# Kernel optimization log

Measured on AMD Instinct MI355X. Metric: run time of the kernel, lower is better.

## Reference

```python
import jax, jax.numpy as jnp
import numpy as np

N_HEAD = 16
N_FEAT = 1024
D_HEAD = N_FEAT // N_HEAD


def setup_inputs() -> dict:
    key = jax.random.key(0)
    ks = jax.random.split(key, 12)
    B, L, T = 8, 128, 64
    s = 0.05
    return {
        "q": jax.random.normal(ks[0], (B, 1, N_FEAT), jnp.float32),
        "kv": jax.random.normal(ks[1], (B, L, T, N_FEAT), jnp.float32),
        "Wq": jax.random.normal(ks[2], (D_HEAD, D_HEAD), jnp.float32) * s,
        "bq": jax.random.normal(ks[3], (D_HEAD,), jnp.float32) * s,
        "Wk": jax.random.normal(ks[4], (D_HEAD, D_HEAD), jnp.float32) * s,
        "bk": jax.random.normal(ks[5], (D_HEAD,), jnp.float32) * s,
        "Wv": jax.random.normal(ks[6], (D_HEAD, D_HEAD), jnp.float32) * s,
        "bv": jax.random.normal(ks[7], (D_HEAD,), jnp.float32) * s,
        "Wo": jax.random.normal(ks[8], (N_FEAT, N_FEAT), jnp.float32) * s,
        "bo": jax.random.normal(ks[9], (N_FEAT,), jnp.float32) * s,
    }


def reference(q, kv, Wq, bq, Wk, bk, Wv, bv, Wo, bo):
    B, L, T, D = kv.shape
    H, dh = N_HEAD, D_HEAD
    # mean-pool q over its singleton length dim and kv over T for keys
    qm = q.mean(axis=-2)                      # [B, D]
    km = kv.mean(axis=-2)                     # [B, L, D]
    qh = qm.reshape(B, H, dh)                 # [B, H, dh]
    kh = km.reshape(B, L, H, dh)              # [B, L, H, dh]
    vh = kv.reshape(B, L, T, H, dh)           # [B, L, T, H, dh]
    # per-head linear projections (torch Linear: x @ W.T + b)
    qh = qh @ Wq.T + bq
    kh = kh @ Wk.T + bk
    vh = vh @ Wv.T + bv
    # faithful transpose chain from the original module
    qh = jnp.swapaxes(qh, -2, -3)             # [H, B, dh]  (3D: swaps B and H)
    kh = jnp.swapaxes(kh, -2, -3)             # [B, H, L, dh]
    # broadcasted matmul -> cross-batch attention [B, H, B, L]
    attw = jnp.matmul(qh, jnp.swapaxes(kh, -1, -2)) / jnp.sqrt(jnp.float32(dh))
    attn = jax.nn.softmax(attw, axis=-1)      # [B, H, B, L]
    # value reshuffle: [B,L,T,H,dh] -> [B,H,T,L,dh] -> [B,H,T,dh,L] -> [B,H,T*dh,L]
    v = jnp.swapaxes(vh, -2, -4)
    v = jnp.swapaxes(v, -1, -2)
    v = v.reshape(B, H, T * dh, L)
    ct = jnp.matmul(attn, jnp.swapaxes(v, -1, -2))   # [B, H, B, T*dh]
    ct = ct.reshape(B, H, B, T, dh)
    ct = jnp.swapaxes(ct, -2, -4)                    # [B, T, B, H, dh]
    ct = ct.reshape(B, T, B, H * dh)                 # [B, T, B, D]
    return ct @ Wo.T + bo
```

## Files before the change

kernel.cpp:

```cpp
#include <hip/hip_runtime.h>
#include <hip/hip_bf16.h>

#define BDIM 8
#define LDIM 128
#define TDIM 64
#define NFEAT 1024
#define HNUM 16
#define DH 64

#define GM 4096
#define GN 1024
#define GK 1024

typedef __attribute__((ext_vector_type(8))) short short8;
typedef __attribute__((ext_vector_type(4))) float f32x4;

__device__ __forceinline__ unsigned short f2bf(float x) {
  union { float f; unsigned u; } v; v.f = x;
  unsigned r = v.u + 0x7fffu + ((v.u >> 16) & 1u);
  return (unsigned short)(r >> 16);
}

__device__ __forceinline__ void gload_lds16(const void* g, void* l) {
  __builtin_amdgcn_global_load_lds((const __attribute__((address_space(1))) void*)g,
                                   (__attribute__((address_space(3))) void*)l, 16, 0, 0);
}

__global__ __launch_bounds__(256) void mean_score_weff_kernel(
    const float* __restrict__ kv, const float* __restrict__ q,
    const float* __restrict__ Wq, const float* __restrict__ bq,
    const float* __restrict__ Wk, const float* __restrict__ Wo,
    const float* __restrict__ Wv, const float* __restrict__ bv,
    const float* __restrict__ bo, float* __restrict__ scores,
    unsigned short* __restrict__ Weff, float* __restrict__ beff) {
  __shared__ float km_s[NFEAT];
  __shared__ float Wk_s[DH * 67];
  __shared__ float kw_s[HNUM * DH];
  __shared__ float wqkw_s[HNUM * 66];
  __shared__ float bqkw_s[HNUM];
  __shared__ float worow[NFEAT];
  __shared__ float red[256];
  const int bl = blockIdx.x;
  const int tid = threadIdx.x;
  const int b1 = bl >> 7, l = bl & 127;

  {
    const float* src = kv + (size_t)bl * (TDIM * NFEAT) + tid * 4;
    float4 acc = make_float4(0.f, 0.f, 0.f, 0.f);
    for (int t0 = 0; t0 < TDIM; t0 += 8) {
      float4 v[8];
#pragma unroll
      for (int jj = 0; jj < 8; ++jj)
        v[jj] = *(const float4*)(src + (t0 + jj) * NFEAT);
#pragma unroll
      for (int jj = 0; jj < 8; ++jj) {
        acc.x += v[jj].x; acc.y += v[jj].y; acc.z += v[jj].z; acc.w += v[jj].w;
      }
    }
    const float s = 1.f / TDIM;
    *(float4*)(km_s + tid * 4) = make_float4(acc.x * s, acc.y * s, acc.z * s, acc.w * s);
  }
#pragma unroll
  for (int rep = 0; rep < 4; ++rep) {
    const int e4 = rep * 256 + tid;
    const int row = e4 >> 4, c4 = e4 & 15;
    const float4 v = *(const float4*)(Wk + row * DH + c4 * 4);
    float* dst = Wk_s + row * 67 + c4 * 4;
    dst[0] = v.x; dst[1] = v.y; dst[2] = v.z; dst[3] = v.w;
  }
  __syncthreads();
#pragma unroll
  for (int rep = 0; rep < 4; ++rep) {
    const int e = rep * 256 + tid;
    const int h = e >> 6, dd = e & 63;
    float acc = 0.f;
#pragma unroll 4
    for (int d = 0; d < DH; ++d) acc += Wk_s[dd * 67 + d] * km_s[h * 64 + d];
    kw_s[h * 64 + dd] = acc;
  }
  __syncthreads();
#pragma unroll
  for (int rep = 0; rep < 4; ++rep) {
    const int e = rep * 256 + tid;
    const int h = e >> 6, i = e & 63;
    float acc = 0.f;
#pragma unroll 4
    for (int dd = 0; dd < DH; ++dd) acc += Wq[dd * DH + i] * kw_s[h * 64 + dd];
    wqkw_s[h * 66 + i] = acc;
  }
  if (tid < HNUM) {
    float acc = 0.f;
#pragma unroll 4
    for (int dd = 0; dd < DH; ++dd) acc += bq[dd] * kw_s[tid * 64 + dd];
    bqkw_s[tid] = acc;
  }
  __syncthreads();
  if (tid < 128) {
    const int h = tid >> 3, b2 = tid & 7;
    const float* qrow = q + b2 * NFEAT + h * DH;
    const float* wrow = wqkw_s + h * 66;
    float acc = 0.f;
#pragma unroll
    for (int i4 = 0; i4 < 16; ++i4) {
      const float4 qv = *(const float4*)(qrow + i4 * 4);
      acc += qv.x * wrow[i4 * 4 + 0] + qv.y * wrow[i4 * 4 + 1] +
             qv.z * wrow[i4 * 4 + 2] + qv.w * wrow[i4 * 4 + 3];
    }
    scores[(((size_t)b1 * HNUM + h) * BDIM + b2) * LDIM + l] =
        (acc + bqkw_s[h]) * 0.125f;
  }
  {
    const int f = bl;
    *(float4*)(worow + tid * 4) = *(const float4*)(Wo + (size_t)f * NFEAT + tid * 4);
    __syncthreads();
    const int g0 = tid * 4;
    const int hbase = (g0 >> 6) << 6;
    const int i0 = g0 & 63;
    float a0 = 0, a1 = 0, a2 = 0, a3 = 0;
#pragma unroll 4
    for (int d = 0; d < DH; ++d) {
      const float wod = worow[hbase + d];
      const float4 wv4 = *(const float4*)(Wv + d * DH + i0);
      a0 += wod * wv4.x; a1 += wod * wv4.y; a2 += wod * wv4.z; a3 += wod * wv4.w;
    }
    ushort4 pk;
    pk.x = f2bf(a0); pk.y = f2bf(a1); pk.z = f2bf(a2); pk.w = f2bf(a3);
    *(ushort4*)(Weff + (size_t)f * NFEAT + g0) = pk;
    red[tid] = worow[g0 + 0] * bv[i0 + 0] + worow[g0 + 1] * bv[i0 + 1] +
               worow[g0 + 2] * bv[i0 + 2] + worow[g0 + 3] * bv[i0 + 3];
    __syncthreads();
    for (int sft = 128; sft > 0; sft >>= 1) {
      if (tid < sft) red[tid] += red[tid + sft];
      __syncthreads();
    }
    if (tid == 0) beff[f] = bo[f] + red[0];
  }
}

#define HSTRIDE 1032
__global__ __launch_bounds__(64) void pool_kernel(
    const float* __restrict__ kv, const float* __restrict__ scores,
    unsigned short* __restrict__ pooled) {
  __shared__ float wlds[4 * HSTRIDE];
  const int b1 = blockIdx.x;
  const int t = blockIdx.y;
  const int ftile = blockIdx.z;
  const int tid = threadIdx.x;
  {
    const int row = tid & 31;
    const int half = tid >> 5;
    const int hloc = row >> 3, b2 = row & 7;
    const float* srow = scores +
        (((size_t)b1 * HNUM + ftile * 4 + hloc) * BDIM + b2) * LDIM + half * 64;
    float4 sv[16];
#pragma unroll
    for (int j = 0; j < 16; ++j) sv[j] = *(const float4*)(srow + j * 4);
    float m = -1e30f;
#pragma unroll
    for (int j = 0; j < 16; ++j)
      m = fmaxf(m, fmaxf(fmaxf(sv[j].x, sv[j].y), fmaxf(sv[j].z, sv[j].w)));
    m = fmaxf(m, __shfl_xor(m, 32, 64));
    float ssum = 0.f;
#pragma unroll
    for (int j = 0; j < 16; ++j) {
      sv[j].x = expf(sv[j].x - m); sv[j].y = expf(sv[j].y - m);
      sv[j].z = expf(sv[j].z - m); sv[j].w = expf(sv[j].w - m);
      ssum += sv[j].x + sv[j].y + sv[j].z + sv[j].w;
    }
    ssum += __shfl_xor(ssum, 32, 64);
    const float inv = 1.f / ssum;
    float* wdst = wlds + hloc * HSTRIDE + b2 * LDIM + half * 64;
#pragma unroll
    for (int j = 0; j < 16; ++j) {
      float4 w4 = make_float4(sv[j].x * inv, sv[j].y * inv, sv[j].z * inv, sv[j].w * inv);
      *(float4*)(wdst + j * 4) = w4;
    }
  }
  __syncthreads();
  const int f = ftile * 256 + tid * 4;
  const int hh = tid >> 4;
  const float* kvbase = kv + ((size_t)b1 * LDIM) * (TDIM * NFEAT) + t * NFEAT + f;
  float4 acc[8];
#pragma unroll
  for (int b2 = 0; b2 < 8; ++b2) acc[b2] = make_float4(0.f, 0.f, 0.f, 0.f);
  const float* wbase = wlds + hh * HSTRIDE;
  for (int l0 = 0; l0 < LDIM; l0 += 8) {
    float4 v[8];
#pragma unroll
    for (int j = 0; j < 8; ++j)
      v[j] = *(const float4*)(kvbase + (size_t)(l0 + j) * (TDIM * NFEAT));
#pragma unroll
    for (int j = 0; j < 8; ++j) {
#pragma unroll
      for (int b2 = 0; b2 < 8; ++b2) {
        const float w = wbase[b2 * LDIM + l0 + j];
        acc[b2].x += w * v[j].x; acc[b2].y += w * v[j].y;
        acc[b2].z += w * v[j].z; acc[b2].w += w * v[j].w;
      }
    }
  }
  unsigned short* obase = pooled + ((size_t)(b1 * TDIM + t) * BDIM) * NFEAT + f;
#pragma unroll
  for (int b2 = 0; b2 < 8; ++b2) {
    ushort4 pk;
    pk.x = f2bf(acc[b2].x); pk.y = f2bf(acc[b2].y);
    pk.z = f2bf(acc[b2].z); pk.w = f2bf(acc[b2].w);
    *(ushort4*)(obase + b2 * NFEAT) = pk;
  }
}

__global__ __launch_bounds__(256) void mfma_gemm(const unsigned short* __restrict__ A,
                                                 const unsigned short* __restrict__ W,
                                                 const float* __restrict__ beff,
                                                 float* __restrict__ out) {
  __shared__ unsigned short As[2][128 * 32];
  __shared__ unsigned short Bs[2][64 * 32];
  const int tid = threadIdx.x;
  const int w = tid >> 6, l = tid & 63;
  const int mBase = blockIdx.y * 128, nBase = blockIdx.x * 64;
  const int wr = w >> 1, wc = w & 1;

  int arow[2], acol[2];
#pragma unroll
  for (int j = 0; j < 2; ++j) {
    const int cid = j * 256 + tid;
    const int r = cid >> 2, c = cid & 3;
    arow[j] = r;
    acol[j] = (c ^ ((r >> 1) & 3)) * 8;
  }
  const int brow = tid >> 2;
  const int bcol = ((tid & 3) ^ ((brow >> 1) & 3)) * 8;

  const int rl = l & 15, ks = l >> 4;
  const int fsel = (ks ^ ((rl >> 1) & 3)) * 16;

  f32x4 acc[4][2] = {};

#pragma unroll
  for (int j = 0; j < 2; ++j)
    gload_lds16(A + (size_t)(mBase + arow[j]) * GK + acol[j],
                (char*)As[0] + (j * 256 + tid) * 16);
  gload_lds16(W + (size_t)(nBase + brow) * GK + bcol, (char*)Bs[0] + tid * 16);
  __syncthreads();

  int cur = 0;
  for (int t = 0; t < GK / 32; ++t) {
    if (t + 1 < GK / 32) {
      const int k0 = (t + 1) * 32;
#pragma unroll
      for (int j = 0; j < 2; ++j)
        gload_lds16(A + (size_t)(mBase + arow[j]) * GK + k0 + acol[j],
                    (char*)As[cur ^ 1] + (j * 256 + tid) * 16);
      gload_lds16(W + (size_t)(nBase + brow) * GK + k0 + bcol,
                  (char*)Bs[cur ^ 1] + tid * 16);
    }
    short8 a[4], b[2];
#pragma unroll
    for (int m = 0; m < 4; ++m)
      a[m] = *(const short8*)((const char*)As[cur] + (wr * 64 + m * 16 + rl) * 64 + fsel);
#pragma unroll
    for (int n = 0; n < 2; ++n)
      b[n] = *(const short8*)((const char*)Bs[cur] + (wc * 32 + n * 16 + rl) * 64 + fsel);
#pragma unroll
    for (int m = 0; m < 4; ++m)
#pragma unroll
      for (int n = 0; n < 2; ++n)
        acc[m][n] = __builtin_amdgcn_mfma_f32_16x16x32_bf16(a[m], b[n], acc[m][n], 0, 0, 0);
    __syncthreads();
    cur ^= 1;
  }

#pragma unroll
  for (int n = 0; n < 2; ++n) {
    const int col = nBase + wc * 32 + n * 16 + rl;
    const float bv = beff[col];
#pragma unroll
    for (int m = 0; m < 4; ++m) {
      const int row0 = mBase + wr * 64 + m * 16 + ks * 4;
#pragma unroll
      for (int j2 = 0; j2 < 4; ++j2)
        out[(size_t)(row0 + j2) * GN + col] = acc[m][n][j2] + bv;
    }
  }
}

extern "C" void kernel_launch(void* const* d_in, const int* in_sizes, int n_in,
                              void* d_out, int out_size, void* d_ws, size_t ws_size,
                              hipStream_t stream) {
  const float* q  = (const float*)d_in[0];
  const float* kv = (const float*)d_in[1];
  const float* Wq = (const float*)d_in[2];
  const float* bq = (const float*)d_in[3];
  const float* Wk = (const float*)d_in[4];
  const float* Wv = (const float*)d_in[6];
  const float* bv = (const float*)d_in[7];
  const float* Wo = (const float*)d_in[8];
  const float* bo = (const float*)d_in[9];
  float* out = (float*)d_out;

  char* ws = (char*)d_ws;
  float*          scores = (float*)ws;
  float*          beff   = (float*)(ws + (1u << 20));
  unsigned short* Weff   = (unsigned short*)(ws + (1u << 20) + (4u << 10));
  unsigned short* pooled = (unsigned short*)(ws + (4u << 20));

  mean_score_weff_kernel<<<BDIM * LDIM, 256, 0, stream>>>(
      kv, q, Wq, bq, Wk, Wo, Wv, bv, bo, scores, Weff, beff);
  pool_kernel<<<dim3(BDIM, TDIM, 4), 64, 0, stream>>>(kv, scores, pooled);
  mfma_gemm<<<dim3(GN / 64, GM / 128), 256, 0, stream>>>(pooled, Weff, beff, out);
}
```

Measured before the change: 138.7 us.

## Fuse attention pooling with output GEMM in one kernel via LDS

Merges the pooling kernel and the bf16 MFMA GEMM into one kernel. Each block computes softmax weights for all heads of one batch, pools two time steps into a 16x1024 bf16 tile in LDS, then multiplies it against Weff read directly from global memory. This drops the pooled intermediate's global write and read plus one kernel launch. In exchange it uses only 256 blocks with large LDS and recomputes softmax per block. The GEMM loses its LDS staging and double buffering, so Weff is read uncoalesced from global or L2 by every block.

```diff
diff --git a/kernel.cpp b/kernel.cpp
--- a/kernel.cpp
+++ b/kernel.cpp
@@ -19,11 +19,6 @@
   union { float f; unsigned u; } v; v.f = x;
   unsigned r = v.u + 0x7fffu + ((v.u >> 16) & 1u);
   return (unsigned short)(r >> 16);
-}
-
-__device__ __forceinline__ void gload_lds16(const void* g, void* l) {
-  __builtin_amdgcn_global_load_lds((const __attribute__((address_space(1))) void*)g,
-                                   (__attribute__((address_space(3))) void*)l, 16, 0, 0);
 }
 
 __global__ __launch_bounds__(256) void mean_score_weff_kernel(
@@ -137,149 +132,98 @@
   }
 }
 
-#define HSTRIDE 1032
-__global__ __launch_bounds__(64) void pool_kernel(
+__global__ __launch_bounds__(512) void pool_gemm_kernel(
     const float* __restrict__ kv, const float* __restrict__ scores,
-    unsigned short* __restrict__ pooled) {
-  __shared__ float wlds[4 * HSTRIDE];
-  const int b1 = blockIdx.x;
-  const int t = blockIdx.y;
-  const int ftile = blockIdx.z;
+    const unsigned short* __restrict__ Weff, const float* __restrict__ beff,
+    float* __restrict__ out) {
+  __shared__ float wlds[16 * 1032];
+  __shared__ unsigned short plds[16 * 1032];
+  const int blk = blockIdx.x;
+  const int b1 = blk >> 5;
+  const int t0 = (blk & 31) * 2;
   const int tid = threadIdx.x;
-  {
-    const int row = tid & 31;
-    const int half = tid >> 5;
-    const int hloc = row >> 3, b2 = row & 7;
-    const float* srow = scores +
-        (((size_t)b1 * HNUM + ftile * 4 + hloc) * BDIM + b2) * LDIM + half * 64;
-    float4 sv[16];
-#pragma unroll
-    for (int j = 0; j < 16; ++j) sv[j] = *(const float4*)(srow + j * 4);
+
+  if (tid < 128) {
+    const int h = tid >> 3, b2 = tid & 7;
+    const float* srow = scores + (((size_t)b1 * HNUM + h) * BDIM + b2) * LDIM;
     float m = -1e30f;
-#pragma unroll
-    for (int j = 0; j < 16; ++j)
-      m = fmaxf(m, fmaxf(fmaxf(sv[j].x, sv[j].y), fmaxf(sv[j].z, sv[j].w)));
-    m = fmaxf(m, __shfl_xor(m, 32, 64));
+    for (int j = 0; j < 32; ++j) {
+      const float4 s4 = *(const float4*)(srow + j * 4);
+      m = fmaxf(m, fmaxf(fmaxf(s4.x, s4.y), fmaxf(s4.z, s4.w)));
+    }
     float ssum = 0.f;
-#pragma unroll
-    for (int j = 0; j < 16; ++j) {
-      sv[j].x = expf(sv[j].x - m); sv[j].y = expf(sv[j].y - m);
-      sv[j].z = expf(sv[j].z - m); sv[j].w = expf(sv[j].w - m);
-      ssum += sv[j].x + sv[j].y + sv[j].z + sv[j].w;
-    }
-    ssum += __shfl_xor(ssum, 32, 64);
+    float* wdst = wlds + h * 1032 + b2 * 129;
+    for (int j = 0; j < 32; ++j) {
+      const float4 s4 = *(const float4*)(srow + j * 4);
+      const float e0 = expf(s4.x - m), e1 = expf(s4.y - m);
+      const float e2 = expf(s4.z - m), e3 = expf(s4.w - m);
+      wdst[j * 4 + 0] = e0; wdst[j * 4 + 1] = e1;
+      wdst[j * 4 + 2] = e2; wdst[j * 4 + 3] = e3;
+      ssum += e0 + e1 + e2 + e3;
+    }
     const float inv = 1.f / ssum;
-    float* wdst = wlds + hloc * HSTRIDE + b2 * LDIM + half * 64;
-#pragma unroll
-    for (int j = 0; j < 16; ++j) {
-      float4 w4 = make_float4(sv[j].x * inv, sv[j].y * inv, sv[j].z * inv, sv[j].w * inv);
-      *(float4*)(wdst + j * 4) = w4;
-    }
-  }
-  __syncthreads();
-  const int f = ftile * 256 + tid * 4;
-  const int hh = tid >> 4;
-  const float* kvbase = kv + ((size_t)b1 * LDIM) * (TDIM * NFEAT) + t * NFEAT + f;
-  float4 acc[8];
-#pragma unroll
-  for (int b2 = 0; b2 < 8; ++b2) acc[b2] = make_float4(0.f, 0.f, 0.f, 0.f);
-  const float* wbase = wlds + hh * HSTRIDE;
-  for (int l0 = 0; l0 < LDIM; l0 += 8) {
-    float4 v[8];
-#pragma unroll
-    for (int j = 0; j < 8; ++j)
-      v[j] = *(const float4*)(kvbase + (size_t)(l0 + j) * (TDIM * NFEAT));
-#pragma unroll
-    for (int j = 0; j < 8; ++j) {
-#pragma unroll
-      for (int b2 = 0; b2 < 8; ++b2) {
-        const float w = wbase[b2 * LDIM + l0 + j];
-        acc[b2].x += w * v[j].x; acc[b2].y += w * v[j].y;
-        acc[b2].z += w * v[j].z; acc[b2].w += w * v[j].w;
+    for (int j = 0; j < 128; ++j) wdst[j] *= inv;
+  }
+  __syncthreads();
+
+  {
+    const int tt = tid >> 8;
+    const int f0 = (tid & 255) * 4;
+    const int hh = f0 >> 6;
+    const float* kvb =
+        kv + (((size_t)b1 * LDIM) * TDIM + (t0 + tt)) * NFEAT + f0;
+    const float* wbase = wlds + hh * 1032;
+    float4 acc[8];
+#pragma unroll
+    for (int b2 = 0; b2 < 8; ++b2) acc[b2] = make_float4(0.f, 0.f, 0.f, 0.f);
+    for (int l0 = 0; l0 < LDIM; l0 += 8) {
+      float4 v[8];
+#pragma unroll
+      for (int j = 0; j < 8; ++j)
+        v[j] = *(const float4*)(kvb + (size_t)(l0 + j) * (TDIM * NFEAT));
+#pragma unroll
+      for (int j = 0; j < 8; ++j) {
+#pragma unroll
+        for (int b2 = 0; b2 < 8; ++b2) {
+          const float w = wbase[b2 * 129 + l0 + j];
+          acc[b2].x += w * v[j].x; acc[b2].y += w * v[j].y;
+          acc[b2].z += w * v[j].z; acc[b2].w += w * v[j].w;
+        }
       }
     }
-  }
-  unsigned short* obase = pooled + ((size_t)(b1 * TDIM + t) * BDIM) * NFEAT + f;
-#pragma unroll
-  for (int b2 = 0; b2 < 8; ++b2) {
-    ushort4 pk;
-    pk.x = f2bf(acc[b2].x); pk.y = f2bf(acc[b2].y);
-    pk.z = f2bf(acc[b2].z); pk.w = f2bf(acc[b2].w);
-    *(ushort4*)(obase + b2 * NFEAT) = pk;
-  }
-}
-
-__global__ __launch_bounds__(256) void mfma_gemm(const unsigned short* __restrict__ A,
-                                                 const unsigned short* __restrict__ W,
-                                                 const float* __restrict__ beff,
-                                                 float* __restrict__ out) {
-  __shared__ unsigned short As[2][128 * 32];
-  __shared__ unsigned short Bs[2][64 * 32];
-  const int tid = threadIdx.x;
-  const int w = tid >> 6, l = tid & 63;
-  const int mBase = blockIdx.y * 128, nBase = blockIdx.x * 64;
-  const int wr = w >> 1, wc = w & 1;
-
-  int arow[2], acol[2];
-#pragma unroll
-  for (int j = 0; j < 2; ++j) {
-    const int cid = j * 256 + tid;
-    const int r = cid >> 2, c = cid & 3;
-    arow[j] = r;
-    acol[j] = (c ^ ((r >> 1) & 3)) * 8;
-  }
-  const int brow = tid >> 2;
-  const int bcol = ((tid & 3) ^ ((brow >> 1) & 3)) * 8;
-
-  const int rl = l & 15, ks = l >> 4;
-  const int fsel = (ks ^ ((rl >> 1) & 3)) * 16;
-
-  f32x4 acc[4][2] = {};
-
-#pragma unroll
-  for (int j = 0; j < 2; ++j)
-    gload_lds16(A + (size_t)(mBase + arow[j]) * GK + acol[j],
-                (char*)As[0] + (j * 256 + tid) * 16);
-  gload_lds16(W + (size_t)(nBase + brow) * GK + bcol, (char*)Bs[0] + tid * 16);
-  __syncthreads();
-
-  int cur = 0;
-  for (int t = 0; t < GK / 32; ++t) {
-    if (t + 1 < GK / 32) {
-      const int k0 = (t + 1) * 32;
-#pragma unroll
-      for (int j = 0; j < 2; ++j)
-        gload_lds16(A + (size_t)(mBase + arow[j]) * GK + k0 + acol[j],
-                    (char*)As[cur ^ 1] + (j * 256 + tid) * 16);
-      gload_lds16(W + (size_t)(nBase + brow) * GK + k0 + bcol,
-                  (char*)Bs[cur ^ 1] + tid * 16);
-    }
-    short8 a[4], b[2];
-#pragma unroll
-    for (int m = 0; m < 4; ++m)
-      a[m] = *(const short8*)((const char*)As[cur] + (wr * 64 + m * 16 + rl) * 64 + fsel);
-#pragma unroll
-    for (int n = 0; n < 2; ++n)
-      b[n] = *(const short8*)((const char*)Bs[cur] + (wc * 32 + n * 16 + rl) * 64 + fsel);
-#pragma unroll
-    for (int m = 0; m < 4; ++m)
-#pragma unroll
-      for (int n = 0; n < 2; ++n)
-        acc[m][n] = __builtin_amdgcn_mfma_f32_16x16x32_bf16(a[m], b[n], acc[m][n], 0, 0, 0);
-    __syncthreads();
-    cur ^= 1;
-  }
-
-#pragma unroll
-  for (int n = 0; n < 2; ++n) {
-    const int col = nBase + wc * 32 + n * 16 + rl;
-    const float bv = beff[col];
-#pragma unroll
-    for (int m = 0; m < 4; ++m) {
-      const int row0 = mBase + wr * 64 + m * 16 + ks * 4;
+#pragma unroll
+    for (int b2 = 0; b2 < 8; ++b2) {
+      ushort4 pk;
+      pk.x = f2bf(acc[b2].x); pk.y = f2bf(acc[b2].y);
+      pk.z = f2bf(acc[b2].z); pk.w = f2bf(acc[b2].w);
+      *(ushort4*)(plds + (tt * 8 + b2) * 1032 + f0) = pk;
+    }
+  }
+  __syncthreads();
+
+  {
+    const int wv = tid >> 6, lane = tid & 63;
+    const int rl = lane & 15, ks = lane >> 4;
+    const int nb = wv * 128;
+    f32x4 gacc[8] = {};
+    for (int k0 = 0; k0 < GK; k0 += 32) {
+      const short8 a =
+          *(const short8*)((const char*)plds + rl * 2064 + (k0 + ks * 8) * 2);
+#pragma unroll
+      for (int n = 0; n < 8; ++n) {
+        const short8 b = *(const short8*)(Weff +
+            (size_t)(nb + n * 16 + rl) * GK + k0 + ks * 8);
+        gacc[n] = __builtin_amdgcn_mfma_f32_16x16x32_bf16(a, b, gacc[n], 0, 0, 0);
+      }
+    }
+    const size_t row0 = (size_t)(b1 * 64 + t0) * 8 + ks * 4;
+#pragma unroll
+    for (int n = 0; n < 8; ++n) {
+      const int col = nb + n * 16 + rl;
+      const float bvv = beff[col];
 #pragma unroll
       for (int j2 = 0; j2 < 4; ++j2)
-        out[(size_t)(row0 + j2) * GN + col] = acc[m][n][j2] + bv;
+        out[(row0 + j2) * GN + col] = gacc[n][j2] + bvv;
     }
   }
 }
@@ -302,10 +246,8 @@
   float*          scores = (float*)ws;
   float*          beff   = (float*)(ws + (1u << 20));
   unsigned short* Weff   = (unsigned short*)(ws + (1u << 20) + (4u << 10));
-  unsigned short* pooled = (unsigned short*)(ws + (4u << 20));
 
   mean_score_weff_kernel<<<BDIM * LDIM, 256, 0, stream>>>(
       kv, q, Wq, bq, Wk, Wo, Wv, bv, bo, scores, Weff, beff);
-  pool_kernel<<<dim3(BDIM, TDIM, 4), 64, 0, stream>>>(kv, scores, pooled);
-  mfma_gemm<<<dim3(GN / 64, GM / 128), 256, 0, stream>>>(pooled, Weff, beff, out);
-}
+  pool_gemm_kernel<<<256, 512, 0, stream>>>(kv, scores, Weff, beff, out);
+}
```

Result: slower. 177.6 us (+28.1%).
